# Kernel tuning notes

Hardware: AMD Instinct MI355X
Metric: run time of the kernel (lower is better)

Reference implementation:

```python
import jax, jax.numpy as jnp
import numpy as np

D_MODEL = 512; D_STATE = 64; D_CONV = 4; EXPAND = 2; HEADDIM = 64
D_INNER = EXPAND * D_MODEL          # 1024
NHEADS = D_INNER // HEADDIM         # 16
D_IN_PROJ = 2 * D_INNER + 2 * D_STATE + NHEADS  # z, xBC, dt
CONV_DIM = D_INNER + 2 * D_STATE
BETA = 0.5
BATCH = 8; SEQLEN = 1024
EPS_LN = 1e-12; EPS_RMS = 1e-5


def layernorm(x, w, b, eps=EPS_LN):
    mu = jnp.mean(x, axis=-1, keepdims=True)
    var = jnp.var(x, axis=-1, keepdims=True)
    return (x - mu) * jax.lax.rsqrt(var + eps) * w + b


def causal_dw_conv(x, w, b):
    # x: (b, l, c); w: (c, d_conv) depthwise; causal left-pad d_conv-1
    xt = jnp.transpose(x, (0, 2, 1))                 # (b, c, l)
    k = w[:, None, :]                                # (c, 1, d_conv)
    y = jax.lax.conv_general_dilated(
        xt, k, window_strides=(1,), padding=[(D_CONV - 1, 0)],
        feature_group_count=CONV_DIM,
        dimension_numbers=('NCH', 'OIH', 'NCH'))
    return jnp.transpose(y, (0, 2, 1)) + b


def ssd(x, dt, A, Bm, Cm, Dp):
    # x: (b,l,h,p)  dt: (b,l,h)  A: (h)  Bm,Cm: (b,l,n)  Dp: (h)
    dA = jnp.exp(dt * A)  # (b,l,h) decay per step

    def step(h, inp):
        dA_t, dt_t, B_t, C_t, x_t = inp
        # h: (b, heads, p, n)
        h = h * dA_t[:, :, None, None] + jnp.einsum('bh,bn,bhp->bhpn', dt_t, B_t, x_t)
        y = jnp.einsum('bhpn,bn->bhp', h, C_t)
        return h, y

    init = jnp.zeros((x.shape[0], NHEADS, HEADDIM, D_STATE), x.dtype)
    xs = (jnp.moveaxis(dA, 1, 0), jnp.moveaxis(dt, 1, 0),
          jnp.moveaxis(Bm, 1, 0), jnp.moveaxis(Cm, 1, 0), jnp.moveaxis(x, 1, 0))
    _, ys = jax.lax.scan(step, init, xs)
    y = jnp.moveaxis(ys, 0, 1)           # (b,l,h,p)
    return y + x * Dp[None, None, :, None]


def mamba2(u, in_proj_w, conv_w, conv_b, dt_bias, A_log, Dp, norm_w, out_proj_w):
    zxbcdt = u @ in_proj_w.T                                   # (b,l,D_IN_PROJ)
    z, xBC, dt = jnp.split(zxbcdt, [D_INNER, D_INNER + CONV_DIM], axis=-1)
    dt = jax.nn.softplus(dt + dt_bias)                          # (b,l,h)
    xBC = jax.nn.silu(causal_dw_conv(xBC, conv_w, conv_b))
    x, Bm, Cm = jnp.split(xBC, [D_INNER, D_INNER + D_STATE], axis=-1)
    x = x.reshape(x.shape[0], x.shape[1], NHEADS, HEADDIM)
    A = -jnp.exp(A_log)
    y = ssd(x, dt, A, Bm, Cm, Dp)
    y = y.reshape(y.shape[0], y.shape[1], D_INNER)
    g = y * jax.nn.silu(z)                                      # gated RMSNorm
    g = g * jax.lax.rsqrt(jnp.mean(g * g, axis=-1, keepdims=True) + EPS_RMS) * norm_w
    return g @ out_proj_w.T


def ffn(x, w1, b1, w2, b2, lnw, lnb):
    h = jax.nn.gelu(x @ w1.T + b1, approximate=False)
    h = h @ w2.T + b2
    return layernorm(h + x, lnw, lnb)


def setup_inputs() -> dict:
    key = jax.random.key(0)
    ks = jax.random.split(key, 12)
    item_emb = jax.random.normal(ks[0], (BATCH, SEQLEN, D_MODEL), jnp.float32)
    item_idx = jnp.zeros((BATCH, SEQLEN), jnp.int32)          # single sequence per row
    flip_index = jnp.arange(SEQLEN - 1, -1, -1, dtype=jnp.int64)
    s = 0.02
    in_proj_w = jax.random.normal(ks[1], (D_IN_PROJ, D_MODEL), jnp.float32) * s
    conv_w = jax.random.uniform(ks[2], (CONV_DIM, D_CONV), jnp.float32, -0.5, 0.5)
    conv_b = jnp.zeros((CONV_DIM,), jnp.float32)
    # dt_bias = inverse softplus of dt ~ U[1e-3, 0.1] in log space (mamba init)
    dt = jnp.exp(jax.random.uniform(ks[3], (NHEADS,), jnp.float32,
                                    np.log(1e-3), np.log(0.1)))
    dt_bias = dt + jnp.log(-jnp.expm1(-dt))
    A_log = jnp.log(jax.random.uniform(ks[4], (NHEADS,), jnp.float32, 1.0, 16.0))
    Dp = jnp.ones((NHEADS,), jnp.float32)
    norm_w = jnp.ones((D_INNER,), jnp.float32)
    out_proj_w = jax.random.normal(ks[5], (D_MODEL, D_INNER), jnp.float32) * s
    ln_w = jnp.ones((D_MODEL,), jnp.float32); ln_b = jnp.zeros((D_MODEL,), jnp.float32)
    ffn_w1 = jax.random.normal(ks[6], (4 * D_MODEL, D_MODEL), jnp.float32) * s
    ffn_b1 = jnp.zeros((4 * D_MODEL,), jnp.float32)
    ffn_w2 = jax.random.normal(ks[7], (D_MODEL, 4 * D_MODEL), jnp.float32) * s
    ffn_b2 = jnp.zeros((D_MODEL,), jnp.float32)
    ffn_ln_w = jnp.ones((D_MODEL,), jnp.float32); ffn_ln_b = jnp.zeros((D_MODEL,), jnp.float32)
    return dict(item_emb=item_emb, item_idx=item_idx, flip_index=flip_index,
                in_proj_w=in_proj_w, conv_w=conv_w, conv_b=conv_b, dt_bias=dt_bias,
                A_log=A_log, Dp=Dp, norm_w=norm_w, out_proj_w=out_proj_w,
                ln_w=ln_w, ln_b=ln_b, ffn_w1=ffn_w1, ffn_b1=ffn_b1,
                ffn_w2=ffn_w2, ffn_b2=ffn_b2, ffn_ln_w=ffn_ln_w, ffn_ln_b=ffn_ln_b)


def reference(item_emb, item_idx, flip_index, in_proj_w, conv_w, conv_b, dt_bias,
              A_log, Dp, norm_w, out_proj_w, ln_w, ln_b,
              ffn_w1, ffn_b1, ffn_w2, ffn_b2, ffn_ln_w, ffn_ln_b):
    # item_idx (seq_idx) is all-zeros -> no state resets; dropout is eval-mode identity.
    params = (in_proj_w, conv_w, conv_b, dt_bias, A_log, Dp, norm_w, out_proj_w)
    fwd = mamba2(item_emb, *params)
    bwd = mamba2(item_emb[:, flip_index, :], *params)   # shared weights, as in source
    h = fwd + bwd * BETA + item_emb
    h = layernorm(h, ln_w, ln_b)
    return ffn(h, ffn_w1, ffn_b1, ffn_w2, ffn_b2, ffn_ln_w, ffn_ln_b)
```

## Files before the change

kernel.cpp:

```cpp
#include <hip/hip_runtime.h>
#include <math.h>

#define SEQ     1024
#define NBATCH  8
#define NTOK    8192
#define DMODEL  512
#define DINNER  1024
#define NHEADS  16
#define DPROJ   2192
#define DPROJP  2304
#define CONVDIM 1152
#define DFFN    2048

typedef short bf16x8 __attribute__((ext_vector_type(8)));
typedef float f32x4  __attribute__((ext_vector_type(4)));

__device__ inline unsigned short f2bf(float f) {
  union { float f; unsigned int u; } v; v.f = f;
  unsigned int u = v.u;
  return (unsigned short)((u + 0x7FFFu + ((u >> 16) & 1u)) >> 16);
}
__device__ inline float bf2f(unsigned short s) {
  union { unsigned int u; float f; } v; v.u = ((unsigned int)s) << 16;
  return v.f;
}

#define GLDS16(g, l)                                                         \
  __builtin_amdgcn_global_load_lds(                                          \
      (const __attribute__((address_space(1))) unsigned int*)(g),            \
      (__attribute__((address_space(3))) unsigned int*)(l), 16, 0, 0)

__global__ __launch_bounds__(256) void cvt_bf16(const float* __restrict__ s,
                                                unsigned short* __restrict__ d, int n) {
  int i = blockIdx.x * 256 + threadIdx.x;
  if (i < n) d[i] = f2bf(s[i]);
}

__global__ __launch_bounds__(256) void cvt_bf16_pad(const float* __restrict__ s,
                                                    unsigned short* __restrict__ d,
                                                    int realrows, int cols, int padrows) {
  int i = blockIdx.x * 256 + threadIdx.x;
  if (i < padrows * cols) {
    int r = i / cols;
    d[i] = (r < realrows) ? f2bf(s[i]) : (unsigned short)0;
  }
}

template <int MODE>
__global__ __launch_bounds__(256)
void gemm_bt(const unsigned short* __restrict__ A, const unsigned short* __restrict__ B,
             void* __restrict__ Cout, const float* __restrict__ bias,
             float* __restrict__ aux, int Ksub, int lda, int Nreal, size_t zstrideC) {
  __shared__ unsigned short sA[2][128 * 32];
  __shared__ unsigned short sB[2][128 * 32];
  const int tid = threadIdx.x;
  const int bx = blockIdx.x, by = blockIdx.y, bz = blockIdx.z;
  const int lane = tid & 63;
  const int wave = tid >> 6;
  const int wm = wave >> 1, wn = wave & 1;
  const int arow = tid >> 2;
  const int acol = (tid & 3) << 3;

  const unsigned short* pA = A + (size_t)(by * 128 + arow) * lda + bz * Ksub + acol;
  const unsigned short* pB = B + (size_t)(bx * 128 + arow) * lda + bz * Ksub + acol;
  const size_t stride64 = (size_t)64 * lda;
  char* sAw[2] = { (char*)&sA[0][0] + wave * 1024, (char*)&sA[1][0] + wave * 1024 };
  char* sBw[2] = { (char*)&sB[0][0] + wave * 1024, (char*)&sB[1][0] + wave * 1024 };

  f32x4 acc[4][4];
#pragma unroll
  for (int i = 0; i < 4; i++)
#pragma unroll
    for (int j = 0; j < 4; j++) { f32x4 z = {0.f, 0.f, 0.f, 0.f}; acc[i][j] = z; }

  GLDS16(pA, sAw[0]);
  GLDS16(pA + stride64, sAw[0] + 4096);
  GLDS16(pB, sBw[0]);
  GLDS16(pB + stride64, sBw[0] + 4096);
  pA += 32; pB += 32;
  __syncthreads();

  const int lrow = lane & 15;
  const int lkq = (lane >> 4) << 3;
  int cur = 0;
  for (int k0 = 0; k0 < Ksub; k0 += 32) {
    if (k0 + 32 < Ksub) {
      const int nxt = cur ^ 1;
      GLDS16(pA, sAw[nxt]);
      GLDS16(pA + stride64, sAw[nxt] + 4096);
      GLDS16(pB, sBw[nxt]);
      GLDS16(pB + stride64, sBw[nxt] + 4096);
      pA += 32; pB += 32;
    }
    bf16x8 af[4], bfr[4];
#pragma unroll
    for (int mi = 0; mi < 4; mi++)
      af[mi] = *(const bf16x8*)&sA[cur][(wm * 64 + mi * 16 + lrow) * 32 + lkq];
#pragma unroll
    for (int ni = 0; ni < 4; ni++)
      bfr[ni] = *(const bf16x8*)&sB[cur][(wn * 64 + ni * 16 + lrow) * 32 + lkq];
#pragma unroll
    for (int mi = 0; mi < 4; mi++)
#pragma unroll
      for (int ni = 0; ni < 4; ni++)
        acc[mi][ni] = __builtin_amdgcn_mfma_f32_16x16x32_bf16(af[mi], bfr[ni], acc[mi][ni], 0, 0, 0);
    __syncthreads();
    cur ^= 1;
  }

  const int row0 = by * 128 + wm * 64;
  const int col0 = bx * 128 + wn * 64;
  float* outf = (float*)Cout;
  unsigned short* outp16 = (unsigned short*)Cout + (size_t)bz * zstrideC;
#pragma unroll
  for (int mi = 0; mi < 4; mi++) {
#pragma unroll
    for (int ni = 0; ni < 4; ni++) {
      const int col = col0 + ni * 16 + lrow;
      if (col < Nreal) {
        const float bval = (MODE == 0 || MODE == 1) && bias ? bias[col] : 0.f;
#pragma unroll
        for (int r = 0; r < 4; r++) {
          const int row = row0 + mi * 16 + ((lane >> 4) << 2) + r;
          float v = acc[mi][ni][r] + bval;
          if (MODE == 1) {
            float g = 0.5f * v * (1.f + erff(v * 0.7071067811865476f));
            ((unsigned short*)Cout)[(size_t)row * Nreal + col] = f2bf(g);
          } else if (MODE == 2) {
            ((unsigned short*)Cout)[(size_t)row * Nreal + col] = f2bf(v);
            if (col >= 2176) aux[(size_t)row * 16 + (col - 2176)] = v;
          } else if (MODE == 3) {
            outp16[(size_t)row * Nreal + col] = f2bf(v);
          } else {
            outf[(size_t)row * Nreal + col] = v;
          }
        }
      }
    }
  }
}

__global__ __launch_bounds__(256)
void dt_softplus(const float* __restrict__ zdt, const float* __restrict__ dt_bias,
                 float* __restrict__ dtf, float* __restrict__ dtb) {
  int i = blockIdx.x * 256 + threadIdx.x;
  int dir = i >> 17;
  int rem = i & 131071;
  int row = rem >> 10;
  int t = rem & 1023;
  int b = row >> 4, h = row & 15;
  int srow = (b << 10) + (dir ? (1023 - t) : t);
  float v = zdt[(size_t)srow * 16 + h] + dt_bias[h];
  float dt = (v > 20.f) ? v : log1pf(expf(v));
  (dir ? dtb : dtf)[(row << 10) + t] = dt;
}

__global__ __launch_bounds__(256)
void conv_silu_bf(const unsigned short* __restrict__ zxb, const float* __restrict__ cw,
                  const float* __restrict__ cb,
                  unsigned short* __restrict__ xcf, unsigned short* __restrict__ xcb) {
  const int tid = threadIdx.x;
  const int c = blockIdx.x * 128 + (tid & 127);
  const int b = blockIdx.y;
  const int seg = blockIdx.z * 2 + (tid >> 7);
  const int t0 = seg << 5;
  const float w0 = cw[c * 4 + 0], w1 = cw[c * 4 + 1], w2 = cw[c * 4 + 2], w3 = cw[c * 4 + 3];
  const float bias = cb[c];
  const unsigned short* src = zxb + (size_t)(b << 10) * DPROJ + DINNER + c;
  unsigned short* dstf = xcf + (size_t)(b << 10) * CONVDIM + c;
  unsigned short* dstb = xcb + (size_t)(b << 10) * CONVDIM + c;
  float r0 = 0.f, r1 = 0.f, r2 = 0.f;
  if (t0 >= 3) {
    r0 = bf2f(src[(size_t)(t0 - 3) * DPROJ]);
    r1 = bf2f(src[(size_t)(t0 - 2) * DPROJ]);
    r2 = bf2f(src[(size_t)(t0 - 1) * DPROJ]);
  }
  for (int s = t0; s < t0 + 32; s++) {
    float x = bf2f(src[(size_t)s * DPROJ]);
    float vf = bias + w0 * r0 + w1 * r1 + w2 * r2 + w3 * x;
    dstf[(size_t)s * CONVDIM] = f2bf(vf / (1.f + expf(-vf)));
    int tp = 1026 - s;
    if (tp <= 1023) {
      float vb = bias + w0 * x + w1 * r2 + w2 * r1 + w3 * r0;
      dstb[(size_t)tp * CONVDIM] = f2bf(vb / (1.f + expf(-vb)));
    }
    r0 = r1; r1 = r2; r2 = x;
  }
  if (seg == 31) {
    float v2 = bias + w1 * r2 + w2 * r1 + w3 * r0;
    float v1 = bias + w2 * r2 + w3 * r1;
    float v0 = bias + w3 * r2;
    dstb[(size_t)2 * CONVDIM] = f2bf(v2 / (1.f + expf(-v2)));
    dstb[(size_t)1 * CONVDIM] = f2bf(v1 / (1.f + expf(-v1)));
    dstb[0] = f2bf(v0 / (1.f + expf(-v0)));
  }
}

__global__ __launch_bounds__(256)
void ssd_chunk(const unsigned short* __restrict__ xcf, const unsigned short* __restrict__ xcb,
               const float* __restrict__ dtf, const float* __restrict__ dtb,
               const float* __restrict__ A_log, const float* __restrict__ Dp,
               unsigned short* __restrict__ yf, unsigned short* __restrict__ yb) {
  const int blk = blockIdx.x;
  const int dir = blk >> 7;
  const int b = (blk >> 4) & 7;
  const int h = blk & 15;
  const unsigned short* xc = dir ? xcb : xcf;
  const float* dts = (dir ? dtb : dtf) + ((size_t)((b << 4) + h) << 10);
  unsigned short* yo = dir ? yb : yf;
  const float A = -expf(A_log[h]);
  const float Dh = Dp[h];
  const int tid = threadIdx.x;
  const int lane = tid & 63;
  const int w = tid >> 6;
  const int lrow = lane & 15;
  const int quad = lane >> 4;
  const int lk8 = quad << 3;
  const int bS = b << 10;
  const int pr = tid & 31;
  const int sg = tid >> 5;

  __shared__ unsigned short Cb[64 * 72];
  __shared__ unsigned short Bb[64 * 72];
  __shared__ unsigned short Xt[64 * 72];
  __shared__ unsigned short Bt[64 * 72];
  __shared__ unsigned short Mb[64 * 72];
  __shared__ unsigned short Hb[64 * 72];
  __shared__ float sdt_all[1024];

  {
    float4 dv = *(const float4*)(dts + tid * 4);
    *(float4*)&sdt_all[tid * 4] = dv;
  }

  f32x4 hacc[4];
#pragma unroll
  for (int j = 0; j < 4; j++) { f32x4 z = {0.f, 0.f, 0.f, 0.f}; hacc[j] = z; }

  for (int c = 0; c < 16; c++) {
    const int t0 = c << 6;
    __syncthreads();

    float dtl = sdt_all[t0 + lane];
    float v = dtl;
#pragma unroll
    for (int off = 1; off < 64; off <<= 1) {
      float o = __shfl_up(v, off);
      if (lane >= off) v += o;
    }
    const float Lv = A * v;
    const float ev = expf(Lv);
    const float LL = __shfl(Lv, 63);
    const float wv = dtl * expf(LL - Lv);
    const float dtot = expf(LL);

#pragma unroll
    for (int j = 0; j < 4; j++)
#pragma unroll
      for (int r = 0; r < 4; r++)
        Hb[(w * 16 + quad * 4 + r) * 72 + j * 16 + lrow] = f2bf(hacc[j][r]);

#pragma unroll
    for (int pass = 0; pass < 2; pass++) {
      int u = pass * 256 + tid;
      int sl = u >> 3, c8 = u & 7;
      const unsigned short* rowp = xc + (size_t)(bS + t0 + sl) * CONVDIM;
      uint4 vb = *(const uint4*)(rowp + 1024 + c8 * 8);
      uint4 vc = *(const uint4*)(rowp + 1088 + c8 * 8);
      *(uint4*)&Bb[sl * 72 + c8 * 8] = vb;
      *(uint4*)&Cb[sl * 72 + c8 * 8] = vc;
    }

    {
      unsigned int xv[8], bv[8];
      const unsigned short* base = xc + (size_t)(bS + t0 + sg * 8) * CONVDIM;
#pragma unroll
      for (int k = 0; k < 8; k++) {
        const unsigned short* rp = base + (size_t)k * CONVDIM;
        xv[k] = *(const unsigned int*)(rp + h * 64 + pr * 2);
        bv[k] = *(const unsigned int*)(rp + 1024 + pr * 2);
      }
      unsigned short x0[8], x1[8], b0[8], b1[8];
#pragma unroll
      for (int k = 0; k < 8; k++) {
        float ws = __shfl(wv, sg * 8 + k);
        x0[k] = (unsigned short)(xv[k] & 0xffff);
        x1[k] = (unsigned short)(xv[k] >> 16);
        b0[k] = f2bf(bf2f((unsigned short)(bv[k] & 0xffff)) * ws);
        b1[k] = f2bf(bf2f((unsigned short)(bv[k] >> 16)) * ws);
      }
      *(uint4*)&Xt[(pr * 2 + 0) * 72 + sg * 8] = *(const uint4*)x0;
      *(uint4*)&Xt[(pr * 2 + 1) * 72 + sg * 8] = *(const uint4*)x1;
      *(uint4*)&Bt[(pr * 2 + 0) * 72 + sg * 8] = *(const uint4*)b0;
      *(uint4*)&Bt[(pr * 2 + 1) * 72 + sg * 8] = *(const uint4*)b1;
    }
    __syncthreads();

    f32x4 m1[4];
#pragma unroll
    for (int j = 0; j < 4; j++) { f32x4 z = {0.f, 0.f, 0.f, 0.f}; m1[j] = z; }
#pragma unroll
    for (int kq = 0; kq < 2; kq++) {
      bf16x8 af = *(const bf16x8*)&Cb[(w * 16 + lrow) * 72 + kq * 32 + lk8];
#pragma unroll
      for (int j = 0; j < 4; j++) {
        bf16x8 bf = *(const bf16x8*)&Bb[(j * 16 + lrow) * 72 + kq * 32 + lk8];
        m1[j] = __builtin_amdgcn_mfma_f32_16x16x32_bf16(af, bf, m1[j], 0, 0, 0);
      }
    }
#pragma unroll
    for (int r = 0; r < 4; r++) {
      int i = w * 16 + quad * 4 + r;
      float Li = __shfl(Lv, i);
#pragma unroll
      for (int j = 0; j < 4; j++) {
        int s = j * 16 + lrow;
        float Ls = __shfl(Lv, s);
        float ds = __shfl(dtl, s);
        float val = (s <= i) ? m1[j][r] * expf(Li - Ls) * ds : 0.f;
        Mb[i * 72 + s] = f2bf(val);
      }
    }
    __syncthreads();

    f32x4 Y[4], T[4], S[4];
#pragma unroll
    for (int j = 0; j < 4; j++) {
      f32x4 z = {0.f, 0.f, 0.f, 0.f};
      Y[j] = z; T[j] = z; S[j] = z;
    }
#pragma unroll
    for (int kq = 0; kq < 2; kq++) {
      bf16x8 am = *(const bf16x8*)&Mb[(w * 16 + lrow) * 72 + kq * 32 + lk8];
      bf16x8 ac = *(const bf16x8*)&Cb[(w * 16 + lrow) * 72 + kq * 32 + lk8];
      bf16x8 ax = *(const bf16x8*)&Xt[(w * 16 + lrow) * 72 + kq * 32 + lk8];
#pragma unroll
      for (int j = 0; j < 4; j++) {
        bf16x8 bx = *(const bf16x8*)&Xt[(j * 16 + lrow) * 72 + kq * 32 + lk8];
        bf16x8 bh = *(const bf16x8*)&Hb[(j * 16 + lrow) * 72 + kq * 32 + lk8];
        bf16x8 bw = *(const bf16x8*)&Bt[(j * 16 + lrow) * 72 + kq * 32 + lk8];
        Y[j] = __builtin_amdgcn_mfma_f32_16x16x32_bf16(am, bx, Y[j], 0, 0, 0);
        T[j] = __builtin_amdgcn_mfma_f32_16x16x32_bf16(ac, bh, T[j], 0, 0, 0);
        S[j] = __builtin_amdgcn_mfma_f32_16x16x32_bf16(ax, bw, S[j], 0, 0, 0);
      }
    }

#pragma unroll
    for (int r = 0; r < 4; r++) {
      int i = w * 16 + quad * 4 + r;
      float ei = __shfl(ev, i);
#pragma unroll
      for (int j = 0; j < 4; j++) {
        int p = j * 16 + lrow;
        float yv = Y[j][r] + ei * T[j][r] + Dh * bf2f(Xt[p * 72 + i]);
        yo[(size_t)(bS + t0 + i) * DINNER + h * 64 + p] = f2bf(yv);
      }
    }
#pragma unroll
    for (int j = 0; j < 4; j++)
#pragma unroll
      for (int r = 0; r < 4; r++)
        hacc[j][r] = dtot * hacc[j][r] + S[j][r];
  }
}

__device__ inline float2 block_sum2_256(float a, float b) {
#pragma unroll
  for (int o = 32; o >= 1; o >>= 1) { a += __shfl_xor(a, o); b += __shfl_xor(b, o); }
  __shared__ float ra[4], rb[4];
  const int lane = threadIdx.x & 63, w = threadIdx.x >> 6;
  if (lane == 0) { ra[w] = a; rb[w] = b; }
  __syncthreads();
  float2 out;
  out.x = ra[0] + ra[1] + ra[2] + ra[3];
  out.y = rb[0] + rb[1] + rb[2] + rb[3];
  return out;
}

__global__ __launch_bounds__(256)
void gate_rms_comb(const unsigned short* __restrict__ yf, const unsigned short* __restrict__ yb,
                   const unsigned short* __restrict__ zxb, const float* __restrict__ nw,
                   unsigned short* __restrict__ comb) {
  const int bt = blockIdx.x;
  const int b = bt >> 10, t = bt & 1023;
  const int zrowb = (b << 10) + (1023 - t);
  const int tid = threadIdx.x;
  ushort4 yf4 = *(const ushort4*)(yf + (size_t)bt * DINNER + tid * 4);
  ushort4 yb4 = *(const ushort4*)(yb + (size_t)bt * DINNER + tid * 4);
  ushort4 zf4 = *(const ushort4*)(zxb + (size_t)bt * DPROJ + tid * 4);
  ushort4 zb4 = *(const ushort4*)(zxb + (size_t)zrowb * DPROJ + tid * 4);
  float gf[4], gb[4];
  {
    float z0 = bf2f(zf4.x), z1 = bf2f(zf4.y), z2 = bf2f(zf4.z), z3 = bf2f(zf4.w);
    gf[0] = bf2f(yf4.x) * (z0 / (1.f + expf(-z0)));
    gf[1] = bf2f(yf4.y) * (z1 / (1.f + expf(-z1)));
    gf[2] = bf2f(yf4.z) * (z2 / (1.f + expf(-z2)));
    gf[3] = bf2f(yf4.w) * (z3 / (1.f + expf(-z3)));
  }
  {
    float z0 = bf2f(zb4.x), z1 = bf2f(zb4.y), z2 = bf2f(zb4.z), z3 = bf2f(zb4.w);
    gb[0] = bf2f(yb4.x) * (z0 / (1.f + expf(-z0)));
    gb[1] = bf2f(yb4.y) * (z1 / (1.f + expf(-z1)));
    gb[2] = bf2f(yb4.z) * (z2 / (1.f + expf(-z2)));
    gb[3] = bf2f(yb4.w) * (z3 / (1.f + expf(-z3)));
  }
  float2 sr = block_sum2_256(gf[0]*gf[0] + gf[1]*gf[1] + gf[2]*gf[2] + gf[3]*gf[3],
                             gb[0]*gb[0] + gb[1]*gb[1] + gb[2]*gb[2] + gb[3]*gb[3]);
  float sf = rsqrtf(sr.x * (1.f / 1024.f) + 1e-5f);
  float sb = 0.5f * rsqrtf(sr.y * (1.f / 1024.f) + 1e-5f);
  float4 wv = *(const float4*)(nw + tid * 4);
  unsigned short* o = comb + (size_t)bt * DINNER + tid * 4;
  o[0] = f2bf((gf[0] * sf + gb[0] * sb) * wv.x);
  o[1] = f2bf((gf[1] * sf + gb[1] * sb) * wv.y);
  o[2] = f2bf((gf[2] * sf + gb[2] * sb) * wv.z);
  o[3] = f2bf((gf[3] * sf + gb[3] * sb) * wv.w);
}

__global__ __launch_bounds__(256)
void combine_ln(const unsigned short* __restrict__ mo, const float* __restrict__ u,
                const float* __restrict__ w, const float* __restrict__ bias,
                float* __restrict__ hln, unsigned short* __restrict__ hbf) {
  const int bt = blockIdx.x;
  const int tid = threadIdx.x;
  const float2 uu = *(const float2*)(u + (size_t)bt * DMODEL + tid * 2);
  float vx = uu.x, vy = uu.y;
#pragma unroll
  for (int z = 0; z < 4; z++) {
    ushort2 p = *(const ushort2*)(mo + (size_t)z * NTOK * DMODEL + (size_t)bt * DMODEL + tid * 2);
    vx += bf2f(p.x);
    vy += bf2f(p.y);
  }
  float2 sr = block_sum2_256(vx + vy, vx * vx + vy * vy);
  float mean = sr.x * (1.f / 512.f);
  float var = sr.y * (1.f / 512.f) - mean * mean;
  float inv = rsqrtf(var + 1e-12f);
  float2 wv = *(const float2*)(w + tid * 2);
  float2 bv = *(const float2*)(bias + tid * 2);
  float ox = (vx - mean) * inv * wv.x + bv.x;
  float oy = (vy - mean) * inv * wv.y + bv.y;
  *(float2*)(hln + (size_t)bt * DMODEL + tid * 2) = make_float2(ox, oy);
  hbf[(size_t)bt * DMODEL + tid * 2] = f2bf(ox);
  hbf[(size_t)bt * DMODEL + tid * 2 + 1] = f2bf(oy);
}

__global__ __launch_bounds__(256)
void final_ln(const unsigned short* __restrict__ f2, const float* __restrict__ b2,
              const float* __restrict__ hln,
              const float* __restrict__ w, const float* __restrict__ bias,
              float* __restrict__ outp) {
  const int bt = blockIdx.x;
  const int tid = threadIdx.x;
  const float2 bb = *(const float2*)(b2 + tid * 2);
  const float2 h = *(const float2*)(hln + (size_t)bt * DMODEL + tid * 2);
  float vx = bb.x + h.x;
  float vy = bb.y + h.y;
#pragma unroll
  for (int z = 0; z < 4; z++) {
    ushort2 p = *(const ushort2*)(f2 + (size_t)z * NTOK * DMODEL + (size_t)bt * DMODEL + tid * 2);
    vx += bf2f(p.x);
    vy += bf2f(p.y);
  }
  float2 sr = block_sum2_256(vx + vy, vx * vx + vy * vy);
  float mean = sr.x * (1.f / 512.f);
  float var = sr.y * (1.f / 512.f) - mean * mean;
  float inv = rsqrtf(var + 1e-12f);
  float2 wv = *(const float2*)(w + tid * 2);
  float2 bv = *(const float2*)(bias + tid * 2);
  *(float2*)(outp + (size_t)bt * DMODEL + tid * 2) =
      make_float2((vx - mean) * inv * wv.x + bv.x, (vy - mean) * inv * wv.y + bv.y);
}

extern "C" void kernel_launch(void* const* d_in, const int* in_sizes, int n_in,
                              void* d_out, int out_size, void* d_ws, size_t ws_size,
                              hipStream_t stream) {
  const float* item_emb   = (const float*)d_in[0];
  const float* in_proj_w  = (const float*)d_in[3];
  const float* conv_w     = (const float*)d_in[4];
  const float* conv_b     = (const float*)d_in[5];
  const float* dt_bias    = (const float*)d_in[6];
  const float* A_log      = (const float*)d_in[7];
  const float* Dp         = (const float*)d_in[8];
  const float* norm_w     = (const float*)d_in[9];
  const float* out_proj_w = (const float*)d_in[10];
  const float* ln_w       = (const float*)d_in[11];
  const float* ln_b       = (const float*)d_in[12];
  const float* w1         = (const float*)d_in[13];
  const float* b1         = (const float*)d_in[14];
  const float* w2         = (const float*)d_in[15];
  const float* b2         = (const float*)d_in[16];
  const float* fln_w      = (const float*)d_in[17];
  const float* fln_b      = (const float*)d_in[18];
  float* outp = (float*)d_out;
  char* ws = (char*)d_ws;

  const size_t o_ubf  = 0;
  const size_t o_win  = 8388608;
  const size_t o_wout = 10747904;
  const size_t o_w1   = 11796480;
  const size_t o_w2   = 13893632;
  const size_t o_dtf  = 15990784;
  const size_t o_dtb  = 16515072;
  const size_t o_zdt  = 17039360;
  const size_t o_zxb  = 17563648;
  const size_t o_xcf  = 53477376;
  const size_t o_xcb  = 72351744;
  const size_t o_yf   = 91226112;
  const size_t o_yb   = 108003328;
  const size_t o_comb = o_xcf;
  const size_t o_mo   = o_zxb;
  const size_t o_hln  = o_yb;
  const size_t o_hbf  = o_ubf;
  const size_t o_h1   = o_xcb;
  const size_t o_f2   = o_zxb;

  unsigned short* u_bf  = (unsigned short*)(ws + o_ubf);
  unsigned short* winb  = (unsigned short*)(ws + o_win);
  unsigned short* woutb = (unsigned short*)(ws + o_wout);
  unsigned short* w1b   = (unsigned short*)(ws + o_w1);
  unsigned short* w2b   = (unsigned short*)(ws + o_w2);
  float* dtf = (float*)(ws + o_dtf);
  float* dtb = (float*)(ws + o_dtb);
  float* zdt = (float*)(ws + o_zdt);
  unsigned short* zxb = (unsigned short*)(ws + o_zxb);
  unsigned short* xcf = (unsigned short*)(ws + o_xcf);
  unsigned short* xcb = (unsigned short*)(ws + o_xcb);
  unsigned short* yf  = (unsigned short*)(ws + o_yf);
  unsigned short* yb  = (unsigned short*)(ws + o_yb);
  unsigned short* comb = (unsigned short*)(ws + o_comb);
  unsigned short* mo  = (unsigned short*)(ws + o_mo);
  float* hln = (float*)(ws + o_hln);
  unsigned short* hbf = (unsigned short*)(ws + o_hbf);
  unsigned short* h1b = (unsigned short*)(ws + o_h1);
  unsigned short* f2  = (unsigned short*)(ws + o_f2);

  {
    int n = NTOK * DMODEL;
    cvt_bf16<<<(n + 255) / 256, 256, 0, stream>>>(item_emb, u_bf, n);
    cvt_bf16_pad<<<(DPROJP * DMODEL + 255) / 256, 256, 0, stream>>>(in_proj_w, winb, DPROJ, DMODEL, DPROJP);
    n = DMODEL * DINNER;
    cvt_bf16<<<(n + 255) / 256, 256, 0, stream>>>(out_proj_w, woutb, n);
    n = DFFN * DMODEL;
    cvt_bf16<<<(n + 255) / 256, 256, 0, stream>>>(w1, w1b, n);
    n = DMODEL * DFFN;
    cvt_bf16<<<(n + 255) / 256, 256, 0, stream>>>(w2, w2b, n);
  }

  gemm_bt<2><<<dim3(DPROJP / 128, NTOK / 128), 256, 0, stream>>>(
      u_bf, winb, zxb, nullptr, zdt, DMODEL, DMODEL, DPROJ, 0);

  dt_softplus<<<1024, 256, 0, stream>>>(zdt, dt_bias, dtf, dtb);
  conv_silu_bf<<<dim3(9, NBATCH, 16), 256, 0, stream>>>(zxb, conv_w, conv_b, xcf, xcb);

  ssd_chunk<<<256, 256, 0, stream>>>(xcf, xcb, dtf, dtb, A_log, Dp, yf, yb);

  gate_rms_comb<<<NTOK, 256, 0, stream>>>(yf, yb, zxb, norm_w, comb);

  gemm_bt<3><<<dim3(DMODEL / 128, NTOK / 128, 4), 256, 0, stream>>>(
      comb, woutb, mo, nullptr, nullptr, DINNER / 4, DINNER, DMODEL,
      (size_t)NTOK * DMODEL);

  combine_ln<<<NTOK, 256, 0, stream>>>(mo, item_emb, ln_w, ln_b, hln, hbf);

  gemm_bt<1><<<dim3(DFFN / 128, NTOK / 128), 256, 0, stream>>>(
      hbf, w1b, h1b, b1, nullptr, DMODEL, DMODEL, DFFN, 0);

  gemm_bt<3><<<dim3(DMODEL / 128, NTOK / 128, 4), 256, 0, stream>>>(
      h1b, w2b, f2, nullptr, nullptr, DFFN / 4, DFFN, DMODEL,
      (size_t)NTOK * DMODEL);

  final_ln<<<NTOK, 256, 0, stream>>>(f2, b2, hln, fln_w, fln_b, outp);

  (void)in_sizes; (void)n_in; (void)out_size; (void)ws_size;
}
```

Measured before the change: 382.5 us.

## Prefetch next chunk's inputs into registers and fold D skip into diagonal

The SSD scan kernel now loads the next 64-token chunk's x, B and C values from global memory into registers while the current chunk computes, ping-ponging between two register sets so load latency is hidden. It also adds the D skip term to the diagonal of the intra-chunk mask matrix, which removes a separate per-element shared-memory read and multiply in the output epilogue. The cost is higher register pressure and possible occupancy loss. Rounding the D term into a bf16 mask entry also changes precision slightly.

```diff
diff --git a/kernel.cpp b/kernel.cpp
--- a/kernel.cpp
+++ b/kernel.cpp
@@ -237,10 +237,36 @@
 #pragma unroll
   for (int j = 0; j < 4; j++) { f32x4 z = {0.f, 0.f, 0.f, 0.f}; hacc[j] = z; }
 
-  for (int c = 0; c < 16; c++) {
+  __syncthreads();
+
+  auto load_raw = [&](int c, uint4& vb0, uint4& vc0, uint4& vb1, uint4& vc1,
+                      unsigned int (&xv)[8], unsigned int (&bv)[8]) {
     const int t0 = c << 6;
-    __syncthreads();
-
+    {
+      int sl = tid >> 3, c8 = tid & 7;
+      const unsigned short* rowp = xc + (size_t)(bS + t0 + sl) * CONVDIM;
+      vb0 = *(const uint4*)(rowp + 1024 + c8 * 8);
+      vc0 = *(const uint4*)(rowp + 1088 + c8 * 8);
+      int u = 256 + tid;
+      sl = u >> 3; c8 = u & 7;
+      rowp = xc + (size_t)(bS + t0 + sl) * CONVDIM;
+      vb1 = *(const uint4*)(rowp + 1024 + c8 * 8);
+      vc1 = *(const uint4*)(rowp + 1088 + c8 * 8);
+    }
+    const unsigned short* base = xc + (size_t)(bS + t0 + sg * 8) * CONVDIM;
+#pragma unroll
+    for (int k = 0; k < 8; k++) {
+      const unsigned short* rp = base + (size_t)k * CONVDIM;
+      xv[k] = *(const unsigned int*)(rp + h * 64 + pr * 2);
+      bv[k] = *(const unsigned int*)(rp + 1024 + pr * 2);
+    }
+  };
+
+  auto step = [&](int c, uint4& vb0, uint4& vc0, uint4& vb1, uint4& vc1,
+                  unsigned int (&xv)[8], unsigned int (&bv)[8],
+                  uint4& nvb0, uint4& nvc0, uint4& nvb1, uint4& nvc1,
+                  unsigned int (&nxv)[8], unsigned int (&nbv)[8]) {
+    const int t0 = c << 6;
     float dtl = sdt_all[t0 + lane];
     float v = dtl;
 #pragma unroll
@@ -254,32 +280,25 @@
     const float wv = dtl * expf(LL - Lv);
     const float dtot = expf(LL);
 
+    __syncthreads();
+
 #pragma unroll
     for (int j = 0; j < 4; j++)
 #pragma unroll
       for (int r = 0; r < 4; r++)
         Hb[(w * 16 + quad * 4 + r) * 72 + j * 16 + lrow] = f2bf(hacc[j][r]);
 
-#pragma unroll
-    for (int pass = 0; pass < 2; pass++) {
-      int u = pass * 256 + tid;
-      int sl = u >> 3, c8 = u & 7;
-      const unsigned short* rowp = xc + (size_t)(bS + t0 + sl) * CONVDIM;
-      uint4 vb = *(const uint4*)(rowp + 1024 + c8 * 8);
-      uint4 vc = *(const uint4*)(rowp + 1088 + c8 * 8);
-      *(uint4*)&Bb[sl * 72 + c8 * 8] = vb;
-      *(uint4*)&Cb[sl * 72 + c8 * 8] = vc;
-    }
-
     {
-      unsigned int xv[8], bv[8];
-      const unsigned short* base = xc + (size_t)(bS + t0 + sg * 8) * CONVDIM;
-#pragma unroll
-      for (int k = 0; k < 8; k++) {
-        const unsigned short* rp = base + (size_t)k * CONVDIM;
-        xv[k] = *(const unsigned int*)(rp + h * 64 + pr * 2);
-        bv[k] = *(const unsigned int*)(rp + 1024 + pr * 2);
-      }
+      int sl = tid >> 3, c8 = tid & 7;
+      *(uint4*)&Bb[sl * 72 + c8 * 8] = vb0;
+      *(uint4*)&Cb[sl * 72 + c8 * 8] = vc0;
+      int u = 256 + tid;
+      sl = u >> 3; c8 = u & 7;
+      *(uint4*)&Bb[sl * 72 + c8 * 8] = vb1;
+      *(uint4*)&Cb[sl * 72 + c8 * 8] = vc1;
+    }
+
+    {
       unsigned short x0[8], x1[8], b0[8], b1[8];
 #pragma unroll
       for (int k = 0; k < 8; k++) {
@@ -294,6 +313,9 @@
       *(uint4*)&Bt[(pr * 2 + 0) * 72 + sg * 8] = *(const uint4*)b0;
       *(uint4*)&Bt[(pr * 2 + 1) * 72 + sg * 8] = *(const uint4*)b1;
     }
+
+    if (c + 1 < 16) load_raw(c + 1, nvb0, nvc0, nvb1, nvc1, nxv, nbv);
+
     __syncthreads();
 
     f32x4 m1[4];
@@ -318,6 +340,7 @@
         float Ls = __shfl(Lv, s);
         float ds = __shfl(dtl, s);
         float val = (s <= i) ? m1[j][r] * expf(Li - Ls) * ds : 0.f;
+        if (s == i) val += Dh;
         Mb[i * 72 + s] = f2bf(val);
       }
     }
@@ -352,7 +375,7 @@
 #pragma unroll
       for (int j = 0; j < 4; j++) {
         int p = j * 16 + lrow;
-        float yv = Y[j][r] + ei * T[j][r] + Dh * bf2f(Xt[p * 72 + i]);
+        float yv = Y[j][r] + ei * T[j][r];
         yo[(size_t)(bS + t0 + i) * DINNER + h * 64 + p] = f2bf(yv);
       }
     }
@@ -361,6 +384,17 @@
 #pragma unroll
       for (int r = 0; r < 4; r++)
         hacc[j][r] = dtot * hacc[j][r] + S[j][r];
+  };
+
+  uint4 vb0A, vc0A, vb1A, vc1A; unsigned int xvA[8], bvA[8];
+  uint4 vb0B, vc0B, vb1B, vc1B; unsigned int xvB[8], bvB[8];
+
+  load_raw(0, vb0A, vc0A, vb1A, vc1A, xvA, bvA);
+  for (int cc = 0; cc < 16; cc += 2) {
+    step(cc,     vb0A, vc0A, vb1A, vc1A, xvA, bvA,
+                 vb0B, vc0B, vb1B, vc1B, xvB, bvB);
+    step(cc + 1, vb0B, vc0B, vb1B, vc1B, xvB, bvB,
+                 vb0A, vc0A, vb1A, vc1A, xvA, bvA);
   }
 }
 
```

Measured after the change: 383.7 us. No clear change (+0.3%).
